# Kernel optimization log

Measured on AMD Instinct MI355X. Metric: run time of the kernel, lower is better.

The kernel has to match this reference:

```python
import jax, jax.numpy as jnp
import numpy as np

ALPHA = 0.1  # entropy regularization coefficient (init kwarg)
S, T, D, A, H = 4096, 500, 6, 3, 64  # simulations, trajectory_length, state_dim, action_dim, baseline/policy hidden


def _mlp(x, W1, b1, W2, b2):
    # x: [..., in]; Linear->ReLU->Linear, matching BaselineModel / policy model
    h = jax.nn.relu(jnp.einsum('...d,hd->...h', x, W1) + b1)
    return jnp.einsum('...h,oh->...o', h, W2) + b2


def setup_inputs() -> dict:
    key = jax.random.key(0)
    ks = jax.random.split(key, 11)
    inp = {
        'trajectories_state_tensor': jax.random.normal(ks[0], (S, D, T), jnp.float32),
        'trajectories_action_tensor': jax.random.normal(ks[1], (S, A, T), jnp.float32),
        'trajectories_reward_tensor': jax.random.normal(ks[2], (S, T), jnp.float32),
        # policy model params (the `model` argument): 6 -> 64 -> 3 MLP
        'pW1': 0.2 * jax.random.normal(ks[3], (H, D), jnp.float32),
        'pb1': jnp.zeros((H,), jnp.float32),
        'pW2': 0.2 * jax.random.normal(ks[4], (A, H), jnp.float32),
        'pb2': jnp.zeros((A,), jnp.float32),
        # baseline params (pretrained stand-in for the embedded Adam loop): 6 -> 64 -> 1
        'bW1': 0.2 * jax.random.normal(ks[5], (H, D), jnp.float32),
        'bb1': jnp.zeros((H,), jnp.float32),
        'bW2': 0.2 * jax.random.normal(ks[6], (1, H), jnp.float32),
        'bb2': jnp.zeros((1,), jnp.float32),
        # MVN covariance sd (init kwarg, constant)
        'sd': 0.25 * jnp.eye(A, dtype=jnp.float32),
    }
    return inp


def reference(trajectories_state_tensor, trajectories_action_tensor,
              trajectories_reward_tensor, pW1, pb1, pW2, pb2,
              bW1, bb1, bW2, bb2, sd):
    st = jnp.transpose(trajectories_state_tensor, (2, 0, 1))   # [T,S,D]
    at = jnp.transpose(trajectories_action_tensor, (2, 0, 1))  # [T,S,A]

    # log N(action | model(state), sd) for every (time, simulation)
    mu = _mlp(st, pW1, pb1, pW2, pb2)                           # [T,S,A]
    L = jnp.linalg.cholesky(sd)                                 # [A,A]
    Linv = jnp.linalg.inv(L)
    z = jnp.einsum('tsa,ba->tsb', at - mu, Linv)                # whitened residual
    a_dim = at.shape[-1]
    ll = (-0.5 * jnp.sum(z * z, axis=-1)
          - jnp.sum(jnp.log(jnp.diagonal(L)))
          - 0.5 * a_dim * jnp.log(2.0 * jnp.pi))                # [T,S]

    # Advantage_estimator: reverse-time cumulative rollout of exp(r) - alpha*loglik
    r_exp = jnp.exp(trajectories_reward_tensor).T               # [T,S]
    g = r_exp - ALPHA * ll
    cum = jnp.flip(jnp.cumsum(jnp.flip(g, axis=0), axis=0), axis=0)  # [T,S]

    # baseline(x) applied to every state column; baseline output subtracted, then detached
    baseline = _mlp(st, bW1, bb1, bW2, bb2)[..., 0]             # [T,S]
    A_hat = jax.lax.stop_gradient(cum - baseline)               # detached advantage

    # expectation[t] = sum(A_hat @ ll[t]) / S ; objective = mean over t
    # = (1/(T*S)) * sum_s (sum_t' A_hat[t',s]) * (sum_t ll[t,s])
    t_len, sims = ll.shape
    out = jnp.dot(A_hat.sum(axis=0), ll.sum(axis=0)) / (t_len * sims)
    return out
```

## Files before the change

kernel.cpp:

```cpp
#include <hip/hip_runtime.h>
#include <math.h>

#define S_SIMS 4096
#define T_LEN  500
#define T_HALF 250
#define D_DIM  6
#define A_DIM  3
#define H_DIM  64
#define ALPHA_C 0.1f
#define NT 4

__global__ __launch_bounds__(256, 4) void mepg_main(
    const float* __restrict__ state,
    const float* __restrict__ action,
    const float* __restrict__ reward,
    const float* __restrict__ pW1, const float* __restrict__ pb1,
    const float* __restrict__ pW2, const float* __restrict__ pb2,
    const float* __restrict__ bW1, const float* __restrict__ bb1,
    const float* __restrict__ bW2, const float* __restrict__ bb2,
    const float* __restrict__ sd,
    float* __restrict__ ASp,
    float* __restrict__ SLp)
{
    __shared__ float wpack[H_DIM * 20];
    const int tid = threadIdx.x;
    if (tid < H_DIM) {
        const int j = tid;
        float* w = &wpack[j * 20];
#pragma unroll
        for (int d = 0; d < D_DIM; ++d) w[d] = pW1[j * D_DIM + d];
        w[6]  = pb1[j];
        w[7]  = pW2[0 * H_DIM + j];
        w[8]  = pW2[1 * H_DIM + j];
        w[9]  = pW2[2 * H_DIM + j];
        w[10] = bb1[j];
        w[11] = bW2[j];
#pragma unroll
        for (int d = 0; d < D_DIM; ++d) w[12 + d] = bW1[j * D_DIM + d];
        w[18] = 0.f; w[19] = 0.f;
    }
    __syncthreads();

    const float s00 = sd[0], s01 = sd[1], s02 = sd[2];
    const float s11 = sd[4], s12 = sd[5], s22 = sd[8];
    const float det = s00 * (s11 * s22 - s12 * s12)
                    - s01 * (s01 * s22 - s12 * s02)
                    + s02 * (s01 * s12 - s11 * s02);
    const float idet = 1.0f / det;
    const float M00 = (s11 * s22 - s12 * s12) * idet;
    const float M01 = (s02 * s12 - s01 * s22) * idet;
    const float M02 = (s01 * s12 - s02 * s11) * idet;
    const float M11 = (s00 * s22 - s02 * s02) * idet;
    const float M12 = (s01 * s02 - s00 * s12) * idet;
    const float M22 = (s00 * s11 - s01 * s01) * idet;
    const float c0 = -0.5f * logf(det) - 0.5f * (float)A_DIM * logf(6.2831853071795864769f);

    const float pb2_0 = pb2[0], pb2_1 = pb2[1], pb2_2 = pb2[2];
    const float bb2_0 = bb2[0];

    const int wave = tid >> 6;
    const int lane = tid & 63;
    const int wid  = blockIdx.x * 4 + wave;
    const int s    = wid >> 1;
    const int half = wid & 1;
    const int tbase = half * T_HALF;

    const float* sbase = state  + (size_t)s * D_DIM * T_LEN + tbase;
    const float* abase = action + (size_t)s * A_DIM * T_LEN + tbase;
    const float* rbase = reward + (size_t)s * T_LEN + tbase;

    float x[D_DIM][NT];
#pragma unroll
    for (int k = 0; k < NT; ++k) {
        const int tl = lane + 64 * k;
        const bool v = (tl < T_HALF);
        const int tc = v ? tl : 0;
#pragma unroll
        for (int d = 0; d < D_DIM; ++d)
            x[d][k] = v ? sbase[d * T_LEN + tc] : 0.f;
    }

    float mu0[NT], mu1[NT], mu2[NT], bl[NT];
#pragma unroll
    for (int k = 0; k < NT; ++k) {
        mu0[k] = pb2_0; mu1[k] = pb2_1; mu2[k] = pb2_2; bl[k] = bb2_0;
    }

#pragma unroll 2
    for (int j = 0; j < H_DIM; ++j) {
        const float4* wp = reinterpret_cast<const float4*>(&wpack[j * 20]);
        const float4 w0 = wp[0];
        const float4 w1 = wp[1];
        const float4 w2 = wp[2];
        const float4 w3 = wp[3];
        const float4 w4 = wp[4];
#pragma unroll
        for (int k = 0; k < NT; ++k) {
            const float pre = fmaf(x[0][k], w0.x, fmaf(x[1][k], w0.y, fmaf(x[2][k], w0.z,
                              fmaf(x[3][k], w0.w, fmaf(x[4][k], w1.x, fmaf(x[5][k], w1.y, w1.z))))));
            const float h = fmaxf(pre, 0.f);
            mu0[k] = fmaf(h, w1.w, mu0[k]);
            mu1[k] = fmaf(h, w2.x, mu1[k]);
            mu2[k] = fmaf(h, w2.y, mu2[k]);
            const float preb = fmaf(x[0][k], w3.x, fmaf(x[1][k], w3.y, fmaf(x[2][k], w3.z,
                               fmaf(x[3][k], w3.w, fmaf(x[4][k], w4.x, fmaf(x[5][k], w4.y, w2.z))))));
            const float hb = fmaxf(preb, 0.f);
            bl[k] = fmaf(hb, w2.w, bl[k]);
        }
    }

    float SL = 0.f;
    float AS = 0.f;
#pragma unroll
    for (int k = 0; k < NT; ++k) {
        const int tl = lane + 64 * k;
        if (tl < T_HALF) {
            const float a0 = abase[0 * T_LEN + tl];
            const float a1 = abase[1 * T_LEN + tl];
            const float a2 = abase[2 * T_LEN + tl];
            const float r  = rbase[tl];
            const float d0 = a0 - mu0[k];
            const float d1 = a1 - mu1[k];
            const float d2 = a2 - mu2[k];
            const float q  = M00 * d0 * d0 + M11 * d1 * d1 + M22 * d2 * d2
                           + 2.f * (M01 * d0 * d1 + M02 * d0 * d2 + M12 * d1 * d2);
            const float ll = -0.5f * q + c0;
            const float g  = __expf(r) - ALPHA_C * ll;
            SL += ll;
            AS += (float)(tbase + tl + 1) * g - bl[k];
        }
    }

#pragma unroll
    for (int o = 32; o > 0; o >>= 1) {
        SL += __shfl_xor(SL, o, 64);
        AS += __shfl_xor(AS, o, 64);
    }
    if (lane == 0) {
        ASp[half * S_SIMS + s] = AS;
        SLp[half * S_SIMS + s] = SL;
    }
}

__global__ __launch_bounds__(1024) void mepg_reduce(
    const float* __restrict__ ASp, const float* __restrict__ SLp,
    float* __restrict__ out)
{
    __shared__ double sh[16];
    double acc = 0.0;
    for (int i = threadIdx.x; i < S_SIMS; i += 1024) {
        const double a = (double)ASp[i] + (double)ASp[S_SIMS + i];
        const double l = (double)SLp[i] + (double)SLp[S_SIMS + i];
        acc += a * l;
    }
#pragma unroll
    for (int o = 32; o > 0; o >>= 1)
        acc += __shfl_xor(acc, o, 64);
    const int w = threadIdx.x >> 6, l = threadIdx.x & 63;
    if (l == 0) sh[w] = acc;
    __syncthreads();
    if (threadIdx.x < 16) {
        double a = sh[threadIdx.x];
#pragma unroll
        for (int o = 8; o > 0; o >>= 1)
            a += __shfl_xor(a, o, 16);
        if (threadIdx.x == 0)
            out[0] = (float)(a / ((double)T_LEN * (double)S_SIMS));
    }
}

extern "C" void kernel_launch(void* const* d_in, const int* in_sizes, int n_in,
                              void* d_out, int out_size, void* d_ws, size_t ws_size,
                              hipStream_t stream) {
    const float* state  = (const float*)d_in[0];
    const float* action = (const float*)d_in[1];
    const float* reward = (const float*)d_in[2];
    const float* pW1    = (const float*)d_in[3];
    const float* pb1    = (const float*)d_in[4];
    const float* pW2    = (const float*)d_in[5];
    const float* pb2    = (const float*)d_in[6];
    const float* bW1    = (const float*)d_in[7];
    const float* bb1    = (const float*)d_in[8];
    const float* bW2    = (const float*)d_in[9];
    const float* bb2    = (const float*)d_in[10];
    const float* sd     = (const float*)d_in[11];

    float* ASp = (float*)d_ws;
    float* SLp = ASp + 2 * S_SIMS;

    dim3 block(256);
    dim3 grid(2 * S_SIMS / 4);
    mepg_main<<<grid, block, 0, stream>>>(state, action, reward,
                                          pW1, pb1, pW2, pb2,
                                          bW1, bb1, bW2, bb2, sd,
                                          ASp, SLp);
    mepg_reduce<<<1, 1024, 0, stream>>>(ASp, SLp, (float*)d_out);
}
```

Before: 177.1 us.

## Pre-pack MLP weights in a separate kernel and read them as wave-uniform scalar loads

After: 177.2 us. No clear change (+0.0%).

```diff
diff --git a/kernel.cpp b/kernel.cpp
--- a/kernel.cpp
+++ b/kernel.cpp
@@ -9,38 +9,41 @@
 #define H_DIM  64
 #define ALPHA_C 0.1f
 #define NT 4
-
-__global__ __launch_bounds__(256, 4) void mepg_main(
-    const float* __restrict__ state,
-    const float* __restrict__ action,
-    const float* __restrict__ reward,
+#define WPK 20
+
+__global__ __launch_bounds__(64) void mepg_pack(
     const float* __restrict__ pW1, const float* __restrict__ pb1,
     const float* __restrict__ pW2, const float* __restrict__ pb2,
     const float* __restrict__ bW1, const float* __restrict__ bb1,
     const float* __restrict__ bW2, const float* __restrict__ bb2,
+    float* __restrict__ wq)
+{
+    const int j = threadIdx.x;
+    float* w = &wq[j * WPK];
+#pragma unroll
+    for (int d = 0; d < D_DIM; ++d) w[d] = pW1[j * D_DIM + d];
+    w[6]  = pb1[j];
+    w[7]  = pW2[0 * H_DIM + j];
+    w[8]  = pW2[1 * H_DIM + j];
+    w[9]  = pW2[2 * H_DIM + j];
+    w[10] = bb1[j];
+    w[11] = bW2[j];
+#pragma unroll
+    for (int d = 0; d < D_DIM; ++d) w[12 + d] = bW1[j * D_DIM + d];
+    w[18] = 0.f; w[19] = 0.f;
+}
+
+__global__ __launch_bounds__(256, 6) void mepg_main(
+    const float* __restrict__ state,
+    const float* __restrict__ action,
+    const float* __restrict__ reward,
+    const float* __restrict__ wq,
+    const float* __restrict__ pb2,
+    const float* __restrict__ bb2,
     const float* __restrict__ sd,
     float* __restrict__ ASp,
     float* __restrict__ SLp)
 {
-    __shared__ float wpack[H_DIM * 20];
-    const int tid = threadIdx.x;
-    if (tid < H_DIM) {
-        const int j = tid;
-        float* w = &wpack[j * 20];
-#pragma unroll
-        for (int d = 0; d < D_DIM; ++d) w[d] = pW1[j * D_DIM + d];
-        w[6]  = pb1[j];
-        w[7]  = pW2[0 * H_DIM + j];
-        w[8]  = pW2[1 * H_DIM + j];
-        w[9]  = pW2[2 * H_DIM + j];
-        w[10] = bb1[j];
-        w[11] = bW2[j];
-#pragma unroll
-        for (int d = 0; d < D_DIM; ++d) w[12 + d] = bW1[j * D_DIM + d];
-        w[18] = 0.f; w[19] = 0.f;
-    }
-    __syncthreads();
-
     const float s00 = sd[0], s01 = sd[1], s02 = sd[2];
     const float s11 = sd[4], s12 = sd[5], s22 = sd[8];
     const float det = s00 * (s11 * s22 - s12 * s12)
@@ -58,6 +61,7 @@
     const float pb2_0 = pb2[0], pb2_1 = pb2[1], pb2_2 = pb2[2];
     const float bb2_0 = bb2[0];
 
+    const int tid  = threadIdx.x;
     const int wave = tid >> 6;
     const int lane = tid & 63;
     const int wid  = blockIdx.x * 4 + wave;
@@ -86,26 +90,25 @@
         mu0[k] = pb2_0; mu1[k] = pb2_1; mu2[k] = pb2_2; bl[k] = bb2_0;
     }
 
-#pragma unroll 2
     for (int j = 0; j < H_DIM; ++j) {
-        const float4* wp = reinterpret_cast<const float4*>(&wpack[j * 20]);
-        const float4 w0 = wp[0];
-        const float4 w1 = wp[1];
-        const float4 w2 = wp[2];
-        const float4 w3 = wp[3];
-        const float4 w4 = wp[4];
+        const float* w = wq + j * WPK;
+        const float w0  = w[0],  w1  = w[1],  w2  = w[2],  w3  = w[3];
+        const float w4  = w[4],  w5  = w[5],  w6  = w[6],  w7  = w[7];
+        const float w8  = w[8],  w9  = w[9],  w10 = w[10], w11 = w[11];
+        const float w12 = w[12], w13 = w[13], w14 = w[14], w15 = w[15];
+        const float w16 = w[16], w17 = w[17];
 #pragma unroll
         for (int k = 0; k < NT; ++k) {
-            const float pre = fmaf(x[0][k], w0.x, fmaf(x[1][k], w0.y, fmaf(x[2][k], w0.z,
-                              fmaf(x[3][k], w0.w, fmaf(x[4][k], w1.x, fmaf(x[5][k], w1.y, w1.z))))));
+            const float pre = fmaf(x[0][k], w0, fmaf(x[1][k], w1, fmaf(x[2][k], w2,
+                              fmaf(x[3][k], w3, fmaf(x[4][k], w4, fmaf(x[5][k], w5, w6))))));
             const float h = fmaxf(pre, 0.f);
-            mu0[k] = fmaf(h, w1.w, mu0[k]);
-            mu1[k] = fmaf(h, w2.x, mu1[k]);
-            mu2[k] = fmaf(h, w2.y, mu2[k]);
-            const float preb = fmaf(x[0][k], w3.x, fmaf(x[1][k], w3.y, fmaf(x[2][k], w3.z,
-                               fmaf(x[3][k], w3.w, fmaf(x[4][k], w4.x, fmaf(x[5][k], w4.y, w2.z))))));
+            mu0[k] = fmaf(h, w7, mu0[k]);
+            mu1[k] = fmaf(h, w8, mu1[k]);
+            mu2[k] = fmaf(h, w9, mu2[k]);
+            const float preb = fmaf(x[0][k], w12, fmaf(x[1][k], w13, fmaf(x[2][k], w14,
+                               fmaf(x[3][k], w15, fmaf(x[4][k], w16, fmaf(x[5][k], w17, w10))))));
             const float hb = fmaxf(preb, 0.f);
-            bl[k] = fmaf(hb, w2.w, bl[k]);
+            bl[k] = fmaf(hb, w11, bl[k]);
         }
     }
 
@@ -187,12 +190,13 @@
 
     float* ASp = (float*)d_ws;
     float* SLp = ASp + 2 * S_SIMS;
+    float* wq  = SLp + 2 * S_SIMS;
+
+    mepg_pack<<<1, 64, 0, stream>>>(pW1, pb1, pW2, pb2, bW1, bb1, bW2, bb2, wq);
 
     dim3 block(256);
     dim3 grid(2 * S_SIMS / 4);
-    mepg_main<<<grid, block, 0, stream>>>(state, action, reward,
-                                          pW1, pb1, pW2, pb2,
-                                          bW1, bb1, bW2, bb2, sd,
-                                          ASp, SLp);
+    mepg_main<<<grid, block, 0, stream>>>(state, action, reward, wq,
+                                          pb2, bb2, sd, ASp, SLp);
     mepg_reduce<<<1, 1024, 0, stream>>>(ASp, SLp, (float*)d_out);
 }
```
